# Kernel tuning notes

Measured on AMD Instinct MI355X. Metric: run time of the kernel, lower is better.

## Reference

```python
import jax, jax.numpy as jnp
import numpy as np
from jax import lax

N_BISECT = 32


def setup_inputs() -> dict:
    key = jax.random.key(0)
    k1, k2 = jax.random.split(key)
    B, D = 128, 1024
    N = 512
    x = jax.random.normal(k1, (B, D), dtype=jnp.float32)
    W = jax.random.normal(k2, (N, D), dtype=jnp.float32)
    lam = jnp.float32(0.5)  # positive scalar
    return {"x": x, "W": W, "lam": lam}


def reference(x, W, lam):
    """Moreau-tropical layer forward.

    For each (b, n): z = W[n] + x[b] (length-D vector). Bisect for tau such
    that sum_d relu(z_d - tau) == lam (N_BISECT fixed steps), then
    delta = sum_d relu(z_d - tau)^2 / (2*lam) and y = tau + delta.
    """
    lam32 = lam.astype(jnp.float32)
    # z: [B, N, D] pairwise sums, computed in fp32 like the Triton kernel
    z = x[:, None, :].astype(jnp.float32) + W[None, :, :].astype(jnp.float32)
    tau_lo = jnp.min(z, axis=-1) - lam32          # [B, N]
    tau_hi = jnp.max(z, axis=-1)                  # [B, N]

    def body(_, carry):
        lo, hi = carry
        mid = 0.5 * (lo + hi)
        f = jnp.sum(jnp.maximum(z - mid[..., None], 0.0), axis=-1)  # [B, N]
        too_low = f > lam32
        lo = jnp.where(too_low, mid, lo)
        hi = jnp.where(too_low, hi, mid)
        return lo, hi

    tau_lo, tau_hi = lax.fori_loop(0, N_BISECT, body, (tau_lo, tau_hi))
    tau = 0.5 * (tau_lo + tau_hi)                 # [B, N] fp32
    slack = jnp.maximum(z - tau[..., None], 0.0)  # [B, N, D]
    delta = jnp.sum(slack * slack, axis=-1) / (2.0 * lam32)  # [B, N]
    y = (tau + delta).astype(x.dtype)
    return y
```

## Files before the change

kernel.cpp:

```cpp
#include <hip/hip_runtime.h>


#define D_DIM   1024
#define TB      8
#define TN      8
#define NPAIR   64
#define NTHR    256
#define SROW    1028
#define CAPP    32
#define NB      16
#define NEG_INF (-3.0e38f)

__global__ void __launch_bounds__(NTHR, 2)
moreau_tropical(const float* __restrict__ x, const float* __restrict__ W,
                const float* __restrict__ lam_p, float* __restrict__ out,
                int B, int N) {
    __shared__ float xs[TB * SROW];
    __shared__ float ws[TN * SROW];
    __shared__ float cand[CAPP * NPAIR];
    __shared__ float pm[16 * 65];
    __shared__ float pmax[NPAIR];
    __shared__ int   pcnt[NPAIR];

    const int tid = threadIdx.x;
    const int dg  = tid & 63;
    const int pos = tid >> 6;
    const int tb  = pos >> 1;
    const int tn  = pos & 1;
    const int b0  = blockIdx.y * TB;
    const int n0  = blockIdx.x * TN;
    const float lam = lam_p[0];

#pragma unroll
    for (int i = 0; i < 8; ++i) {
        const int flat = tid + NTHR * i;
        const int row  = flat >> 8;
        const int c4   = (flat & 255) << 2;
        const int gb   = min(b0 + row, B - 1);
        const int gn   = min(n0 + row, N - 1);
        *(float4*)&xs[row * SROW + c4] = *(const float4*)(x + (size_t)gb * D_DIM + c4);
        *(float4*)&ws[row * SROW + c4] = *(const float4*)(W + (size_t)gn * D_DIM + c4);
    }
    if (tid < NPAIR) pcnt[tid] = 0;
    __syncthreads();

    float m[16];
#pragma unroll
    for (int q = 0; q < 16; ++q) m[q] = NEG_INF;

#pragma unroll
    for (int k = 0; k < 4; ++k) {
        const int col = (k * 64 + dg) * 4;
        float4 xv[4], wv[4];
#pragma unroll
        for (int i = 0; i < 4; ++i) xv[i] = *(const float4*)&xs[(tb * 4 + i) * SROW + col];
#pragma unroll
        for (int j = 0; j < 4; ++j) wv[j] = *(const float4*)&ws[(tn * 4 + j) * SROW + col];
#pragma unroll
        for (int i = 0; i < 4; ++i)
#pragma unroll
            for (int j = 0; j < 4; ++j) {
                const float4 a = xv[i], c = wv[j];
                const float z0 = a.x + c.x, z1 = a.y + c.y;
                const float z2 = a.z + c.z, z3 = a.w + c.w;
                m[i * 4 + j] = fmaxf(m[i * 4 + j],
                                     fmaxf(fmaxf(z0, z1), fmaxf(z2, z3)));
            }
    }

#pragma unroll
    for (int q = 0; q < 16; ++q) {
        m[q] = fmaxf(m[q], __shfl_xor(m[q], 1, 64));
        m[q] = fmaxf(m[q], __shfl_xor(m[q], 2, 64));
    }
    if ((dg & 3) == 0) {
        const int gg = dg >> 2;
#pragma unroll
        for (int i = 0; i < 4; ++i)
#pragma unroll
            for (int j = 0; j < 4; ++j)
                pm[gg * 65 + (tb * 4 + i) * 8 + tn * 4 + j] = m[i * 4 + j];
    }
    __syncthreads();

    if (tid < NPAIR) {
        float v = pm[tid];
#pragma unroll
        for (int g = 1; g < 16; ++g) v = fmaxf(v, pm[g * 65 + tid]);
        pmax[tid] = v;
    }
    __syncthreads();

    float thr[16];
    float tmin[4];
#pragma unroll
    for (int i = 0; i < 4; ++i) {
#pragma unroll
        for (int j = 0; j < 4; ++j)
            thr[i * 4 + j] = pmax[(tb * 4 + i) * 8 + tn * 4 + j] - lam;
        tmin[i] = fminf(fminf(thr[i * 4], thr[i * 4 + 1]),
                        fminf(thr[i * 4 + 2], thr[i * 4 + 3]));
    }

#pragma unroll
    for (int k = 0; k < 4; ++k) {
        const int col = (k * 64 + dg) * 4;
        float4 xv[4], wv[4];
#pragma unroll
        for (int i = 0; i < 4; ++i) xv[i] = *(const float4*)&xs[(tb * 4 + i) * SROW + col];
#pragma unroll
        for (int j = 0; j < 4; ++j) wv[j] = *(const float4*)&ws[(tn * 4 + j) * SROW + col];
#pragma unroll
        for (int i = 0; i < 4; ++i) {
            float g4[4];
#pragma unroll
            for (int j = 0; j < 4; ++j) {
                const float4 a = xv[i], c = wv[j];
                g4[j] = fmaxf(fmaxf(a.x + c.x, a.y + c.y),
                              fmaxf(a.z + c.z, a.w + c.w));
            }
            const float gi = fmaxf(fmaxf(g4[0], g4[1]), fmaxf(g4[2], g4[3]));
            if (gi > tmin[i]) {
#pragma unroll
                for (int j = 0; j < 4; ++j) {
                    const float t = thr[i * 4 + j];
                    if (g4[j] > t) {
                        const float4 a = xv[i], c = wv[j];
                        const int pr = (tb * 4 + i) * 8 + tn * 4 + j;
                        const float z0 = a.x + c.x, z1 = a.y + c.y;
                        const float z2 = a.z + c.z, z3 = a.w + c.w;
                        if (z0 > t) { int s_ = atomicAdd(&pcnt[pr], 1); if (s_ < CAPP) cand[s_ * NPAIR + pr] = z0; }
                        if (z1 > t) { int s_ = atomicAdd(&pcnt[pr], 1); if (s_ < CAPP) cand[s_ * NPAIR + pr] = z1; }
                        if (z2 > t) { int s_ = atomicAdd(&pcnt[pr], 1); if (s_ < CAPP) cand[s_ * NPAIR + pr] = z2; }
                        if (z3 > t) { int s_ = atomicAdd(&pcnt[pr], 1); if (s_ < CAPP) cand[s_ * NPAIR + pr] = z3; }
                    }
                }
            }
        }
    }
    __syncthreads();

    if (tid < NPAIR) {
        const int p  = tid;
        const int pb = p >> 3;
        const int pn = p & 7;
        const int K  = pcnt[p];
        const float M   = pmax[p];
        const float thr0 = M - lam;
        float tau, delta;

        if (K <= CAPP) {
            int Kw = K;
#pragma unroll
            for (int o = 1; o < 64; o <<= 1) Kw = max(Kw, __shfl_xor(Kw, o, 64));

            float lo = thr0, hi = M;
            for (int it = 0; it < NB; ++it) {
                const float mid = 0.5f * (lo + hi);
                float f = 0.0f;
                for (int j = 0; j < Kw; ++j) {
                    float v = cand[j * NPAIR + p];
                    v = (j < K) ? v : NEG_INF;
                    f += fmaxf(v - mid, 0.0f);
                }
                if (f > lam) lo = mid; else hi = mid;
            }
            tau = 0.5f * (lo + hi);
            float s2 = 0.0f;
            for (int j = 0; j < Kw; ++j) {
                float v = cand[j * NPAIR + p];
                v = (j < K) ? v : NEG_INF;
                const float t = fmaxf(v - tau, 0.0f);
                s2 += t * t;
            }
            delta = s2 / (2.0f * lam);
        } else {
            const float* xr = &xs[pb * SROW];
            const float* wr = &ws[pn * SROW];
            float lo = thr0, hi = M;
            for (int it = 0; it < NB; ++it) {
                const float mid = 0.5f * (lo + hi);
                float f = 0.0f;
                for (int d = 0; d < D_DIM; ++d)
                    f += fmaxf(xr[d] + wr[d] - mid, 0.0f);
                if (f > lam) lo = mid; else hi = mid;
            }
            tau = 0.5f * (lo + hi);
            float s2 = 0.0f;
            for (int d = 0; d < D_DIM; ++d) {
                const float t = fmaxf(xr[d] + wr[d] - tau, 0.0f);
                s2 += t * t;
            }
            delta = s2 / (2.0f * lam);
        }

        const int ob = min(b0 + pb, B - 1);
        const int on = min(n0 + pn, N - 1);
        out[(size_t)ob * N + on] = tau + delta;
    }
}

extern "C" void kernel_launch(void* const* d_in, const int* in_sizes, int n_in,
                              void* d_out, int out_size, void* d_ws, size_t ws_size,
                              hipStream_t stream) {
    const float* x    = (const float*)d_in[0];
    const float* W    = (const float*)d_in[1];
    const float* lamp = (const float*)d_in[2];
    float* out        = (float*)d_out;

    const int B = in_sizes[0] / D_DIM;
    const int N = in_sizes[1] / D_DIM;

    dim3 grid((N + TN - 1) / TN, (B + TB - 1) / TB);
    moreau_tropical<<<grid, NTHR, 0, stream>>>(x, W, lamp, out, B, N);
}
```

Baseline: 99.61 us.

## Drop shared-memory staging of x/W rows and read directly from global

Removes the LDS copies of the x and W tiles and loads float4 values straight from global memory (relying on L1/L2), which cuts LDS usage enough to raise launch bounds to 4 blocks per SM. The max reduction now uses full-wave shuffles instead of a shared partial buffer plus an extra barrier. The candidate-collection pass reloads values from global only for the (pair, lane) entries whose per-lane max exceeds the threshold. In exchange the kernel depends on cache hits for repeated global reads, and the rare fallback path now scans global memory.

Result: slower. 119.3 us (+19.8%).

```diff
diff --git a/kernel.cpp b/kernel.cpp
--- a/kernel.cpp
+++ b/kernel.cpp
@@ -6,43 +6,37 @@
 #define TN      8
 #define NPAIR   64
 #define NTHR    256
-#define SROW    1028
 #define CAPP    32
 #define NB      16
 #define NEG_INF (-3.0e38f)
 
-__global__ void __launch_bounds__(NTHR, 2)
+__global__ void __launch_bounds__(NTHR, 4)
 moreau_tropical(const float* __restrict__ x, const float* __restrict__ W,
                 const float* __restrict__ lam_p, float* __restrict__ out,
                 int B, int N) {
-    __shared__ float xs[TB * SROW];
-    __shared__ float ws[TN * SROW];
     __shared__ float cand[CAPP * NPAIR];
-    __shared__ float pm[16 * 65];
     __shared__ float pmax[NPAIR];
     __shared__ int   pcnt[NPAIR];
 
-    const int tid = threadIdx.x;
-    const int dg  = tid & 63;
-    const int pos = tid >> 6;
-    const int tb  = pos >> 1;
-    const int tn  = pos & 1;
-    const int b0  = blockIdx.y * TB;
-    const int n0  = blockIdx.x * TN;
+    const int tid  = threadIdx.x;
+    const int lane = tid & 63;
+    const int wq   = tid >> 6;
+    const int tb   = wq >> 1;
+    const int tn   = wq & 1;
+    const int b0   = blockIdx.y * TB;
+    const int n0   = blockIdx.x * TN;
     const float lam = lam_p[0];
 
+    if (tid < NPAIR) pcnt[tid] = 0;
+
+    const float* xr[4];
+    const float* wr[4];
 #pragma unroll
-    for (int i = 0; i < 8; ++i) {
-        const int flat = tid + NTHR * i;
-        const int row  = flat >> 8;
-        const int c4   = (flat & 255) << 2;
-        const int gb   = min(b0 + row, B - 1);
-        const int gn   = min(n0 + row, N - 1);
-        *(float4*)&xs[row * SROW + c4] = *(const float4*)(x + (size_t)gb * D_DIM + c4);
-        *(float4*)&ws[row * SROW + c4] = *(const float4*)(W + (size_t)gn * D_DIM + c4);
-    }
-    if (tid < NPAIR) pcnt[tid] = 0;
-    __syncthreads();
+    for (int i = 0; i < 4; ++i)
+        xr[i] = x + (size_t)min(b0 + tb * 4 + i, B - 1) * D_DIM + lane * 4;
+#pragma unroll
+    for (int j = 0; j < 4; ++j)
+        wr[j] = W + (size_t)min(n0 + tn * 4 + j, N - 1) * D_DIM + lane * 4;
 
     float m[16];
 #pragma unroll
@@ -50,12 +44,11 @@
 
 #pragma unroll
     for (int k = 0; k < 4; ++k) {
-        const int col = (k * 64 + dg) * 4;
         float4 xv[4], wv[4];
 #pragma unroll
-        for (int i = 0; i < 4; ++i) xv[i] = *(const float4*)&xs[(tb * 4 + i) * SROW + col];
+        for (int i = 0; i < 4; ++i) xv[i] = *(const float4*)(xr[i] + k * 256);
 #pragma unroll
-        for (int j = 0; j < 4; ++j) wv[j] = *(const float4*)&ws[(tn * 4 + j) * SROW + col];
+        for (int j = 0; j < 4; ++j) wv[j] = *(const float4*)(wr[j] + k * 256);
 #pragma unroll
         for (int i = 0; i < 4; ++i)
 #pragma unroll
@@ -70,71 +63,30 @@
 
 #pragma unroll
     for (int q = 0; q < 16; ++q) {
-        m[q] = fmaxf(m[q], __shfl_xor(m[q], 1, 64));
-        m[q] = fmaxf(m[q], __shfl_xor(m[q], 2, 64));
-    }
-    if ((dg & 3) == 0) {
-        const int gg = dg >> 2;
+        float v = m[q];
 #pragma unroll
-        for (int i = 0; i < 4; ++i)
-#pragma unroll
-            for (int j = 0; j < 4; ++j)
-                pm[gg * 65 + (tb * 4 + i) * 8 + tn * 4 + j] = m[i * 4 + j];
+        for (int o = 1; o < 64; o <<= 1) v = fmaxf(v, __shfl_xor(v, o, 64));
+        if (lane == 0)
+            pmax[(tb * 4 + (q >> 2)) * 8 + tn * 4 + (q & 3)] = v;
     }
     __syncthreads();
 
-    if (tid < NPAIR) {
-        float v = pm[tid];
 #pragma unroll
-        for (int g = 1; g < 16; ++g) v = fmaxf(v, pm[g * 65 + tid]);
-        pmax[tid] = v;
-    }
-    __syncthreads();
-
-    float thr[16];
-    float tmin[4];
+    for (int q = 0; q < 16; ++q) {
+        const int i = q >> 2, j = q & 3;
+        const int p = (tb * 4 + i) * 8 + tn * 4 + j;
+        const float thr = pmax[p] - lam;
+        if (m[q] > thr) {
 #pragma unroll
-    for (int i = 0; i < 4; ++i) {
-#pragma unroll
-        for (int j = 0; j < 4; ++j)
-            thr[i * 4 + j] = pmax[(tb * 4 + i) * 8 + tn * 4 + j] - lam;
-        tmin[i] = fminf(fminf(thr[i * 4], thr[i * 4 + 1]),
-                        fminf(thr[i * 4 + 2], thr[i * 4 + 3]));
-    }
-
-#pragma unroll
-    for (int k = 0; k < 4; ++k) {
-        const int col = (k * 64 + dg) * 4;
-        float4 xv[4], wv[4];
-#pragma unroll
-        for (int i = 0; i < 4; ++i) xv[i] = *(const float4*)&xs[(tb * 4 + i) * SROW + col];
-#pragma unroll
-        for (int j = 0; j < 4; ++j) wv[j] = *(const float4*)&ws[(tn * 4 + j) * SROW + col];
-#pragma unroll
-        for (int i = 0; i < 4; ++i) {
-            float g4[4];
-#pragma unroll
-            for (int j = 0; j < 4; ++j) {
-                const float4 a = xv[i], c = wv[j];
-                g4[j] = fmaxf(fmaxf(a.x + c.x, a.y + c.y),
-                              fmaxf(a.z + c.z, a.w + c.w));
-            }
-            const float gi = fmaxf(fmaxf(g4[0], g4[1]), fmaxf(g4[2], g4[3]));
-            if (gi > tmin[i]) {
-#pragma unroll
-                for (int j = 0; j < 4; ++j) {
-                    const float t = thr[i * 4 + j];
-                    if (g4[j] > t) {
-                        const float4 a = xv[i], c = wv[j];
-                        const int pr = (tb * 4 + i) * 8 + tn * 4 + j;
-                        const float z0 = a.x + c.x, z1 = a.y + c.y;
-                        const float z2 = a.z + c.z, z3 = a.w + c.w;
-                        if (z0 > t) { int s_ = atomicAdd(&pcnt[pr], 1); if (s_ < CAPP) cand[s_ * NPAIR + pr] = z0; }
-                        if (z1 > t) { int s_ = atomicAdd(&pcnt[pr], 1); if (s_ < CAPP) cand[s_ * NPAIR + pr] = z1; }
-                        if (z2 > t) { int s_ = atomicAdd(&pcnt[pr], 1); if (s_ < CAPP) cand[s_ * NPAIR + pr] = z2; }
-                        if (z3 > t) { int s_ = atomicAdd(&pcnt[pr], 1); if (s_ < CAPP) cand[s_ * NPAIR + pr] = z3; }
-                    }
-                }
+            for (int k = 0; k < 4; ++k) {
+                const float4 a = *(const float4*)(xr[i] + k * 256);
+                const float4 c = *(const float4*)(wr[j] + k * 256);
+                const float z0 = a.x + c.x, z1 = a.y + c.y;
+                const float z2 = a.z + c.z, z3 = a.w + c.w;
+                if (z0 > thr) { int s_ = atomicAdd(&pcnt[p], 1); if (s_ < CAPP) cand[s_ * NPAIR + p] = z0; }
+                if (z1 > thr) { int s_ = atomicAdd(&pcnt[p], 1); if (s_ < CAPP) cand[s_ * NPAIR + p] = z1; }
+                if (z2 > thr) { int s_ = atomicAdd(&pcnt[p], 1); if (s_ < CAPP) cand[s_ * NPAIR + p] = z2; }
+                if (z3 > thr) { int s_ = atomicAdd(&pcnt[p], 1); if (s_ < CAPP) cand[s_ * NPAIR + p] = z3; }
             }
         }
     }
@@ -145,7 +97,7 @@
         const int pb = p >> 3;
         const int pn = p & 7;
         const int K  = pcnt[p];
-        const float M   = pmax[p];
+        const float M    = pmax[p];
         const float thr0 = M - lam;
         float tau, delta;
 
@@ -175,20 +127,20 @@
             }
             delta = s2 / (2.0f * lam);
         } else {
-            const float* xr = &xs[pb * SROW];
-            const float* wr = &ws[pn * SROW];
+            const float* xrow = x + (size_t)min(b0 + pb, B - 1) * D_DIM;
+            const float* wrow = W + (size_t)min(n0 + pn, N - 1) * D_DIM;
             float lo = thr0, hi = M;
             for (int it = 0; it < NB; ++it) {
                 const float mid = 0.5f * (lo + hi);
                 float f = 0.0f;
                 for (int d = 0; d < D_DIM; ++d)
-                    f += fmaxf(xr[d] + wr[d] - mid, 0.0f);
+                    f += fmaxf(xrow[d] + wrow[d] - mid, 0.0f);
                 if (f > lam) lo = mid; else hi = mid;
             }
             tau = 0.5f * (lo + hi);
             float s2 = 0.0f;
             for (int d = 0; d < D_DIM; ++d) {
-                const float t = fmaxf(xr[d] + wr[d] - tau, 0.0f);
+                const float t = fmaxf(xrow[d] + wrow[d] - tau, 0.0f);
                 s2 += t * t;
             }
             delta = s2 / (2.0f * lam);
```
